# Kernel optimization log

Measured on AMD Instinct MI355X. Metric: run time of the kernel, lower is better.

The kernel has to match this reference:

```python
import jax, jax.numpy as jnp
import numpy as np
import math

B, T, D, H = 2, 2048, 1024, 16


def _layernorm(x, gamma, beta, eps=1e-5):
    mu = jnp.mean(x, axis=-1, keepdims=True)
    var = jnp.var(x, axis=-1, keepdims=True)
    return (x - mu) * jax.lax.rsqrt(var + eps) * gamma + beta


def setup_inputs() -> dict:
    key = jax.random.key(0)
    ks = jax.random.split(key, 12)
    s = 1.0 / math.sqrt(D)
    return {
        "x": jax.random.normal(ks[0], (B, T, D), dtype=jnp.float32),
        "src_mask": jax.random.randint(ks[1], (B, T, T), 0, 2, dtype=jnp.int32),
        "ln_gamma": jnp.ones((D,), jnp.float32),
        "ln_beta": jnp.zeros((D,), jnp.float32),
        "Wq": jax.random.normal(ks[2], (D, D), jnp.float32) * s,
        "bq": jnp.zeros((D,), jnp.float32),
        "Wk": jax.random.normal(ks[3], (D, D), jnp.float32) * s,
        "bk": jnp.zeros((D,), jnp.float32),
        "Wv": jax.random.normal(ks[4], (D, D), jnp.float32) * s,
        "bv": jnp.zeros((D,), jnp.float32),
        "Wo": jax.random.normal(ks[5], (D, D), jnp.float32) * s,
        "bo": jnp.zeros((D,), jnp.float32),
    }


def reference(x, src_mask, ln_gamma, ln_beta, Wq, bq, Wk, bk, Wv, bv, Wo, bo):
    Bx, Tx, Dx = x.shape
    dh = Dx // H
    xn = _layernorm(x, ln_gamma, ln_beta)  # single LN; the three calls are identical
    q = (xn @ Wq + bq).reshape(Bx, Tx, H, dh)
    k = (xn @ Wk + bk).reshape(Bx, Tx, H, dh)
    v = (xn @ Wv + bv).reshape(Bx, Tx, H, dh)
    # scores: B, n, m, h
    attn = jnp.einsum('bnhd,bmhd->bnmh', q, k) / math.sqrt(dh)
    attn = attn + (1.0 - src_mask.astype(attn.dtype))[..., None] * -100000.0
    weight = jax.nn.softmax(attn, axis=2)
    y = jnp.einsum('bnmh,bmhd->bnhd', weight, v).reshape(Bx, Tx, Dx)
    return x + (y @ Wo + bo)
```

## Files before the change

### kernel.cpp

```cpp
#include <hip/hip_runtime.h>
#include <hip/hip_bf16.h>
#include <stdint.h>

#define Tq 2048
#define Dd 1024
#define Hh 16

typedef unsigned short u16;
typedef __attribute__((ext_vector_type(8))) short short8;
typedef __attribute__((ext_vector_type(4))) float f32x4;

__device__ __forceinline__ u16 f2bf(float f) {
  union { float f; unsigned u; } v; v.f = f;
  unsigned r = (v.u + 0x7fffu + ((v.u >> 16) & 1u)) >> 16;
  return (u16)r;
}

__device__ __forceinline__ unsigned pk2bf(float a, float b) {
  __hip_bfloat162 h = __float22bfloat162_rn(float2{a, b});
  union { __hip_bfloat162 h; unsigned u; } c; c.h = h;
  return c.u;
}

__device__ __forceinline__ void load_lds16(const void* g, void* l) {
  __builtin_amdgcn_global_load_lds(
      (const __attribute__((address_space(1))) unsigned*)g,
      (__attribute__((address_space(3))) unsigned*)l, 16, 0, 0);
}

__device__ __forceinline__ f32x4 mfma16(short8 a, short8 b, f32x4 c) {
  return __builtin_amdgcn_mfma_f32_16x16x32_bf16(a, b, c, 0, 0, 0);
}

__global__ __launch_bounds__(256) void prep_kernel(
    const float* __restrict__ x, const float* __restrict__ gamma,
    const float* __restrict__ beta, u16* __restrict__ xn,
    const float* __restrict__ W0, const float* __restrict__ W1,
    const float* __restrict__ W2, const float* __restrict__ W3,
    u16* __restrict__ o_qkv, u16* __restrict__ o_o,
    const int* __restrict__ mask, uint32_t* __restrict__ bits,
    const float* __restrict__ bq, const float* __restrict__ bk,
    const float* __restrict__ bv, float* __restrict__ bias3) {
  __shared__ float t[32][33];
  int idx = blockIdx.x;
  int tid = threadIdx.x;
  if (idx < 4096) {
    int row = idx;
    const float4 v = ((const float4*)(x + (size_t)row * Dd))[tid];
    float s = v.x + v.y + v.z + v.w;
    float s2 = v.x * v.x + v.y * v.y + v.z * v.z + v.w * v.w;
#pragma unroll
    for (int off = 1; off < 64; off <<= 1) {
      s += __shfl_xor(s, off);
      s2 += __shfl_xor(s2, off);
    }
    int w = tid >> 6;
    if ((tid & 63) == 0) { t[0][w] = s; t[0][4 + w] = s2; }
    __syncthreads();
    s = t[0][0] + t[0][1] + t[0][2] + t[0][3];
    s2 = t[0][4] + t[0][5] + t[0][6] + t[0][7];
    float mu = s * (1.0f / Dd);
    float var = s2 * (1.0f / Dd) - mu * mu;
    float rstd = rsqrtf(var + 1e-5f);
    const float4 g = ((const float4*)gamma)[tid];
    const float4 bb = ((const float4*)beta)[tid];
    union { unsigned us[2]; uint2 u2; } o;
    o.us[0] = pk2bf((v.x - mu) * rstd * g.x + bb.x, (v.y - mu) * rstd * g.y + bb.y);
    o.us[1] = pk2bf((v.z - mu) * rstd * g.z + bb.z, (v.w - mu) * rstd * g.w + bb.w);
    *(uint2*)(xn + (size_t)row * Dd + tid * 4) = o.u2;
  } else if (idx < 8192) {
    int ti = idx - 4096;
    int z = ti >> 10, i = ti & 1023;
    const float* W = (z == 0) ? W0 : (z == 1) ? W1 : (z == 2) ? W2 : W3;
    u16* out = (z < 3) ? (o_qkv + (size_t)z * 1024 * 1024) : o_o;
    int k0 = (i & 31) * 32, n0 = (i >> 5) * 32;
    int tx = tid & 31, ty = tid >> 5;
#pragma unroll
    for (int j = 0; j < 4; ++j)
      t[ty + j * 8][tx] = W[(size_t)(k0 + ty + j * 8) * Dd + n0 + tx];
    __syncthreads();
#pragma unroll
    for (int j = 0; j < 4; ++j)
      out[(size_t)(n0 + ty + j * 8) * Dd + k0 + tx] = f2bf(t[tx][ty + j * 8]);
  } else if (idx < 9216) {
    int m = idx - 8192;
    int b = m >> 9, rest = m & 511;
    int qw = rest >> 3, kblk = rest & 7;
    int k = kblk * 256 + tid;
    const int* mp = mask + ((size_t)b * Tq + qw * 32) * Tq + k;
    uint32_t wv = 0;
#pragma unroll
    for (int j = 0; j < 32; ++j) wv |= (mp[(size_t)j * Tq] ? 1u : 0u) << j;
    bits[((size_t)b * 64 + qw) * Tq + k] = wv;
  } else {
    int i = (idx - 9216) * 256 + tid;
    float v = (i < 1024) ? bq[i] : (i < 2048) ? bk[i - 1024] : bv[i - 2048];
    bias3[i] = v;
  }
}

__global__ __launch_bounds__(256) void vt_kernel(
    const u16* __restrict__ qkv, u16* __restrict__ vt) {
  __shared__ u16 t[32][33];
  int bh = blockIdx.z;
  int b = bh >> 4, h = bh & 15;
  int t0 = blockIdx.x * 32, d0 = blockIdx.y * 32;
  int tx = threadIdx.x & 31, ty = threadIdx.x >> 5;
#pragma unroll
  for (int i = 0; i < 4; ++i)
    t[ty + i * 8][tx] =
        qkv[(size_t)(b * Tq + t0 + ty + i * 8) * 3072 + 2048 + h * 64 + d0 + tx];
  __syncthreads();
#pragma unroll
  for (int i = 0; i < 4; ++i)
    vt[((size_t)bh * 64 + d0 + ty + i * 8) * Tq + t0 + tx] = t[tx][ty + i * 8];
}

template <int MODE, int MT>
__global__ __launch_bounds__(256) void gemm_bt(
    const u16* __restrict__ A, const u16* __restrict__ Bt,
    const float* __restrict__ bias, const float* __restrict__ resid,
    void* __restrict__ Cout, int ldc, int K) {
  constexpr int MTI = MT / 32;
  constexpr int ACALLS = MT / 64;
  __shared__ u16 As[MT * 32];
  __shared__ u16 Bs[128 * 32];
  int tid = threadIdx.x;
  int lane = tid & 63, w = tid >> 6;
  int l16 = lane & 15, quad = lane >> 4;
  int wm = w >> 1, wn = w & 1;
  int m0 = blockIdx.y * MT, n0 = blockIdx.x * 128;
  int srow = lane >> 2, scol = (lane & 3) << 3;
  const u16* ga0 = A + (size_t)(m0 + srow) * K + scol;
  const u16* gb0 = Bt + (size_t)(n0 + srow) * K + scol;
  f32x4 acc[MTI][4];
#pragma unroll
  for (int i = 0; i < MTI; ++i)
#pragma unroll
    for (int j = 0; j < 4; ++j) acc[i][j] = {0.f, 0.f, 0.f, 0.f};

  for (int k0 = 0; k0 < K; k0 += 32) {
    __syncthreads();
#pragma unroll
    for (int c = 0; c < ACALLS; ++c) {
      int rb = w * (MT / 4) + c * 16;
      load_lds16(ga0 + (size_t)rb * K + k0, (char*)As + rb * 64);
    }
#pragma unroll
    for (int c = 0; c < 2; ++c) {
      int rb = w * 32 + c * 16;
      load_lds16(gb0 + (size_t)rb * K + k0, (char*)Bs + rb * 64);
    }
    __syncthreads();
    short8 af[MTI], bf[4];
#pragma unroll
    for (int mt = 0; mt < MTI; ++mt)
      af[mt] = *(const short8*)&As[(wm * (MT / 2) + mt * 16 + l16) * 32 + quad * 8];
#pragma unroll
    for (int nt = 0; nt < 4; ++nt)
      bf[nt] = *(const short8*)&Bs[(wn * 64 + nt * 16 + l16) * 32 + quad * 8];
#pragma unroll
    for (int mt = 0; mt < MTI; ++mt)
#pragma unroll
      for (int nt = 0; nt < 4; ++nt)
        acc[mt][nt] = mfma16(af[mt], bf[nt], acc[mt][nt]);
  }
#pragma unroll
  for (int nt = 0; nt < 4; ++nt) {
    int col = n0 + wn * 64 + nt * 16 + l16;
    float bv = bias[col];
    float scl = (MODE == 0 && col < 1024) ? 0.125f : 1.0f;
#pragma unroll
    for (int mt = 0; mt < MTI; ++mt) {
#pragma unroll
      for (int r = 0; r < 4; ++r) {
        int row = m0 + wm * (MT / 2) + mt * 16 + quad * 4 + r;
        size_t idx = (size_t)row * ldc + col;
        float vv = (acc[mt][nt][r] + bv) * scl;
        if (MODE == 0)
          ((u16*)Cout)[idx] = f2bf(vv);
        else
          ((float*)Cout)[idx] = vv + resid[idx];
      }
    }
  }
}

__global__ __launch_bounds__(256, 2) void attn_kernel(
    const u16* __restrict__ qkv, const u16* __restrict__ vt,
    const uint32_t* __restrict__ mbits, u16* __restrict__ ybuf) {
  __shared__ u16 Ks[2][64 * 64];
  __shared__ u16 Vs[2][64 * 64];
  __shared__ u16 Plds[4][32 * 64];
  int tid = threadIdx.x;
  int lane = tid & 63, w = tid >> 6;
  int l16 = lane & 15, quad = lane >> 4;
  int x7 = l16 & 7;
  int qt = blockIdx.x, h = blockIdx.y, b = blockIdx.z;
  int qbase = qt * 128 + w * 32;
  const u16* Qb = qkv + (size_t)b * Tq * 3072 + h * 64;
  const u16* Kb = Qb + 1024;
  const u16* Vb = vt + ((size_t)(b * Hh + h)) * 64 * Tq;
  const uint32_t* Mrow = mbits + ((size_t)b * 64 + (qbase >> 5)) * Tq;
  u16* Pw = Plds[w];

  int half = (w & 1) * 32;
  int r8 = lane >> 3;
  int phys = lane & 7;
  int chunk = phys ^ r8;
  bool isK = (w < 2);

  short8 qf[2][2];
#pragma unroll
  for (int nt = 0; nt < 2; ++nt)
#pragma unroll
    for (int ks = 0; ks < 2; ++ks)
      qf[nt][ks] = *(const short8*)&Qb[(size_t)(qbase + nt * 16 + l16) * 3072 +
                                       ks * 32 + quad * 8];

  f32x4 acc[2][4];
#pragma unroll
  for (int i = 0; i < 2; ++i)
#pragma unroll
    for (int j = 0; j < 4; ++j) acc[i][j] = {0.f, 0.f, 0.f, 0.f};
  float lst[2] = {0.f, 0.f};

  auto stage = [&](int buf, int k0) {
    if (isK) {
#pragma unroll
      for (int j = 0; j < 4; ++j)
        load_lds16(Kb + (size_t)(k0 + half + j * 8 + r8) * 3072 + chunk * 8,
                   (char*)&Ks[buf][0] + (half + j * 8) * 128);
    } else {
#pragma unroll
      for (int j = 0; j < 4; ++j)
        load_lds16(Vb + (size_t)(half + j * 8 + r8) * Tq + k0 + chunk * 8,
                   (char*)&Vs[buf][0] + (half + j * 8) * 128);
    }
  };

  stage(0, 0);

  for (int kt = 0; kt < 32; ++kt) {
    int k0 = kt * 64;
    int buf = kt & 1;
    __syncthreads();
    uint32_t mv[4][4];
#pragma unroll
    for (int mt = 0; mt < 4; ++mt) {
      uint4 m4 = *(const uint4*)&Mrow[k0 + mt * 16 + quad * 4];
      mv[mt][0] = m4.x; mv[mt][1] = m4.y; mv[mt][2] = m4.z; mv[mt][3] = m4.w;
    }
    if (kt < 31) stage(buf ^ 1, k0 + 64);
    const u16* Kt = Ks[buf];
    const u16* Vtile = Vs[buf];
    f32x4 s[4][2];
#pragma unroll
    for (int i = 0; i < 4; ++i)
#pragma unroll
      for (int j = 0; j < 2; ++j) s[i][j] = {0.f, 0.f, 0.f, 0.f};
#pragma unroll
    for (int mt = 0; mt < 4; ++mt)
#pragma unroll
      for (int ks = 0; ks < 2; ++ks) {
        short8 kf = *(const short8*)&Kt[(mt * 16 + l16) * 64 +
                                        (((ks << 2) | quad) ^ x7) * 8];
#pragma unroll
        for (int nt = 0; nt < 2; ++nt)
          s[mt][nt] = mfma16(kf, qf[nt][ks], s[mt][nt]);
      }
#pragma unroll
    for (int nt = 0; nt < 2; ++nt) {
      int shift = nt * 16 + l16;
#pragma unroll
      for (int mt = 0; mt < 4; ++mt) {
#pragma unroll
        for (int r = 0; r < 4; ++r) {
          float sv = ((mv[mt][r] >> shift) & 1u) ? s[mt][nt][r] : -100000.0f;
          float p = __expf(sv);
          s[mt][nt][r] = p;
          lst[nt] += p;
        }
        union { unsigned us[2]; uint2 u2; } pk;
        pk.us[0] = pk2bf(s[mt][nt][0], s[mt][nt][1]);
        pk.us[1] = pk2bf(s[mt][nt][2], s[mt][nt][3]);
        int p16 = (mt * 2 + (quad >> 1)) ^ x7;
        *(uint2*)&Pw[(nt * 16 + l16) * 64 + p16 * 8 + (quad & 1) * 4] = pk.u2;
      }
    }
    short8 pf[2][2];
#pragma unroll
    for (int mt2 = 0; mt2 < 2; ++mt2)
#pragma unroll
      for (int ks = 0; ks < 2; ++ks)
        pf[mt2][ks] = *(const short8*)&Pw[(mt2 * 16 + l16) * 64 +
                                          (((ks << 2) | quad) ^ x7) * 8];
#pragma unroll
    for (int ks = 0; ks < 2; ++ks)
#pragma unroll
      for (int nt2 = 0; nt2 < 4; ++nt2) {
        short8 vf = *(const short8*)&Vtile[(nt2 * 16 + l16) * 64 +
                                           (((ks << 2) | quad) ^ x7) * 8];
#pragma unroll
        for (int mt2 = 0; mt2 < 2; ++mt2)
          acc[mt2][nt2] = mfma16(pf[mt2][ks], vf, acc[mt2][nt2]);
      }
  }
#pragma unroll
  for (int nt = 0; nt < 2; ++nt) {
    lst[nt] += __shfl_xor(lst[nt], 16);
    lst[nt] += __shfl_xor(lst[nt], 32);
  }
#pragma unroll
  for (int mt2 = 0; mt2 < 2; ++mt2)
#pragma unroll
    for (int r = 0; r < 4; ++r) {
      float li = 1.0f / __shfl(lst[mt2], quad * 4 + r);
      size_t row = (size_t)b * Tq + qbase + mt2 * 16 + quad * 4 + r;
#pragma unroll
      for (int nt2 = 0; nt2 < 4; ++nt2)
        ybuf[row * Dd + h * 64 + nt2 * 16 + l16] = f2bf(acc[mt2][nt2][r] * li);
    }
}

extern "C" void kernel_launch(void* const* d_in, const int* in_sizes, int n_in,
                              void* d_out, int out_size, void* d_ws, size_t ws_size,
                              hipStream_t stream) {
  (void)in_sizes; (void)n_in; (void)out_size; (void)ws_size;
  const float* x = (const float*)d_in[0];
  const int* mask = (const int*)d_in[1];
  const float* gamma = (const float*)d_in[2];
  const float* beta = (const float*)d_in[3];
  const float* Wq = (const float*)d_in[4];
  const float* bq = (const float*)d_in[5];
  const float* Wk = (const float*)d_in[6];
  const float* bk = (const float*)d_in[7];
  const float* Wv = (const float*)d_in[8];
  const float* bv = (const float*)d_in[9];
  const float* Wo = (const float*)d_in[10];
  const float* bo = (const float*)d_in[11];
  float* out = (float*)d_out;
  char* ws = (char*)d_ws;

  constexpr size_t SZ_XN = (size_t)4096 * 1024 * 2;
  constexpr size_t SZ_WTQ = (size_t)3072 * 1024 * 2;
  constexpr size_t SZ_WOT = (size_t)1024 * 1024 * 2;
  constexpr size_t SZ_B3 = 3072 * 4;
  constexpr size_t SZ_QKV = (size_t)4096 * 3072 * 2;
  constexpr size_t SZ_MBITS = (size_t)2 * 64 * 2048 * 4;
  constexpr size_t SZ_VT = (size_t)2 * 16 * 64 * 2048 * 2;
  size_t off = 0;
  u16* xn = (u16*)(ws + off); off += SZ_XN;
  u16* wtqkv = (u16*)(ws + off); off += SZ_WTQ;
  u16* wot = (u16*)(ws + off); off += SZ_WOT;
  float* bias3 = (float*)(ws + off); off += SZ_B3;
  u16* qkvb = (u16*)(ws + off); off += SZ_QKV;
  uint32_t* mbits = (uint32_t*)(ws + off); off += SZ_MBITS;
  u16* vtb = (u16*)(ws + off); off += SZ_VT;
  u16* ybuf = (u16*)(ws + off);

  prep_kernel<<<dim3(9228), dim3(256), 0, stream>>>(
      x, gamma, beta, xn, Wq, Wk, Wv, Wo, wtqkv, wot, mask, mbits, bq, bk, bv,
      bias3);
  gemm_bt<0, 128><<<dim3(24, 32), dim3(256), 0, stream>>>(
      xn, wtqkv, bias3, nullptr, qkvb, 3072, 1024);
  vt_kernel<<<dim3(64, 2, 32), dim3(256), 0, stream>>>(qkvb, vtb);
  attn_kernel<<<dim3(16, 16, 2), dim3(256), 0, stream>>>(qkvb, vtb, mbits, ybuf);
  gemm_bt<1, 64><<<dim3(8, 64), dim3(256), 0, stream>>>(
      ybuf, wot, bo, x, out, 1024, 1024);
}
```

Measured before the change: 245.5 us.

## Halve attention query tile per block, use exp2 with folded scale and bitmask select

```diff
diff --git a/kernel.cpp b/kernel.cpp
--- a/kernel.cpp
+++ b/kernel.cpp
@@ -169,7 +169,7 @@
   for (int nt = 0; nt < 4; ++nt) {
     int col = n0 + wn * 64 + nt * 16 + l16;
     float bv = bias[col];
-    float scl = (MODE == 0 && col < 1024) ? 0.125f : 1.0f;
+    float scl = (MODE == 0 && col < 1024) ? 0.18033688011112042f : 1.0f;
 #pragma unroll
     for (int mt = 0; mt < MTI; ++mt) {
 #pragma unroll
@@ -186,22 +186,24 @@
   }
 }
 
-__global__ __launch_bounds__(256, 2) void attn_kernel(
+__global__ __launch_bounds__(256, 4) void attn_kernel(
     const u16* __restrict__ qkv, const u16* __restrict__ vt,
     const uint32_t* __restrict__ mbits, u16* __restrict__ ybuf) {
   __shared__ u16 Ks[2][64 * 64];
   __shared__ u16 Vs[2][64 * 64];
-  __shared__ u16 Plds[4][32 * 64];
+  __shared__ u16 Plds[4][16 * 64];
   int tid = threadIdx.x;
   int lane = tid & 63, w = tid >> 6;
   int l16 = lane & 15, quad = lane >> 4;
   int x7 = l16 & 7;
   int qt = blockIdx.x, h = blockIdx.y, b = blockIdx.z;
-  int qbase = qt * 128 + w * 32;
+  int qbase = qt * 64 + w * 16;
   const u16* Qb = qkv + (size_t)b * Tq * 3072 + h * 64;
   const u16* Kb = Qb + 1024;
   const u16* Vb = vt + ((size_t)(b * Hh + h)) * 64 * Tq;
   const uint32_t* Mrow = mbits + ((size_t)b * 64 + (qbase >> 5)) * Tq;
+  int shift = (qbase & 31) + l16;
+  int shl = 31 - shift;
   u16* Pw = Plds[w];
 
   int half = (w & 1) * 32;
@@ -210,20 +212,15 @@
   int chunk = phys ^ r8;
   bool isK = (w < 2);
 
-  short8 qf[2][2];
-#pragma unroll
-  for (int nt = 0; nt < 2; ++nt)
-#pragma unroll
-    for (int ks = 0; ks < 2; ++ks)
-      qf[nt][ks] = *(const short8*)&Qb[(size_t)(qbase + nt * 16 + l16) * 3072 +
-                                       ks * 32 + quad * 8];
-
-  f32x4 acc[2][4];
-#pragma unroll
-  for (int i = 0; i < 2; ++i)
-#pragma unroll
-    for (int j = 0; j < 4; ++j) acc[i][j] = {0.f, 0.f, 0.f, 0.f};
-  float lst[2] = {0.f, 0.f};
+  short8 qf[2];
+#pragma unroll
+  for (int ks = 0; ks < 2; ++ks)
+    qf[ks] = *(const short8*)&Qb[(size_t)(qbase + l16) * 3072 + ks * 32 + quad * 8];
+
+  f32x4 acc[4];
+#pragma unroll
+  for (int j = 0; j < 4; ++j) acc[j] = {0.f, 0.f, 0.f, 0.f};
+  float lsa[4] = {0.f, 0.f, 0.f, 0.f};
 
   auto stage = [&](int buf, int k0) {
     if (isK) {
@@ -254,73 +251,57 @@
     if (kt < 31) stage(buf ^ 1, k0 + 64);
     const u16* Kt = Ks[buf];
     const u16* Vtile = Vs[buf];
-    f32x4 s[4][2];
-#pragma unroll
-    for (int i = 0; i < 4; ++i)
-#pragma unroll
-      for (int j = 0; j < 2; ++j) s[i][j] = {0.f, 0.f, 0.f, 0.f};
+    f32x4 s[4];
+#pragma unroll
+    for (int i = 0; i < 4; ++i) s[i] = {0.f, 0.f, 0.f, 0.f};
 #pragma unroll
     for (int mt = 0; mt < 4; ++mt)
 #pragma unroll
       for (int ks = 0; ks < 2; ++ks) {
         short8 kf = *(const short8*)&Kt[(mt * 16 + l16) * 64 +
                                         (((ks << 2) | quad) ^ x7) * 8];
-#pragma unroll
-        for (int nt = 0; nt < 2; ++nt)
-          s[mt][nt] = mfma16(kf, qf[nt][ks], s[mt][nt]);
+        s[mt] = mfma16(kf, qf[ks], s[mt]);
       }
 #pragma unroll
-    for (int nt = 0; nt < 2; ++nt) {
-      int shift = nt * 16 + l16;
-#pragma unroll
-      for (int mt = 0; mt < 4; ++mt) {
-#pragma unroll
-        for (int r = 0; r < 4; ++r) {
-          float sv = ((mv[mt][r] >> shift) & 1u) ? s[mt][nt][r] : -100000.0f;
-          float p = __expf(sv);
-          s[mt][nt][r] = p;
-          lst[nt] += p;
-        }
-        union { unsigned us[2]; uint2 u2; } pk;
-        pk.us[0] = pk2bf(s[mt][nt][0], s[mt][nt][1]);
-        pk.us[1] = pk2bf(s[mt][nt][2], s[mt][nt][3]);
-        int p16 = (mt * 2 + (quad >> 1)) ^ x7;
-        *(uint2*)&Pw[(nt * 16 + l16) * 64 + p16 * 8 + (quad & 1) * 4] = pk.u2;
+    for (int mt = 0; mt < 4; ++mt) {
+#pragma unroll
+      for (int r = 0; r < 4; ++r) {
+        float p = __builtin_amdgcn_exp2f(s[mt][r]);
+        int keep = (int)(mv[mt][r] << shl) >> 31;
+        union { float f; int i; } u; u.f = p; u.i &= keep;
+        s[mt][r] = u.f;
+        lsa[r] += u.f;
       }
-    }
-    short8 pf[2][2];
-#pragma unroll
-    for (int mt2 = 0; mt2 < 2; ++mt2)
-#pragma unroll
-      for (int ks = 0; ks < 2; ++ks)
-        pf[mt2][ks] = *(const short8*)&Pw[(mt2 * 16 + l16) * 64 +
-                                          (((ks << 2) | quad) ^ x7) * 8];
+      union { unsigned us[2]; uint2 u2; } pk;
+      pk.us[0] = pk2bf(s[mt][0], s[mt][1]);
+      pk.us[1] = pk2bf(s[mt][2], s[mt][3]);
+      int p16 = (mt * 2 + (quad >> 1)) ^ x7;
+      *(uint2*)&Pw[l16 * 64 + p16 * 8 + (quad & 1) * 4] = pk.u2;
+    }
+    short8 pf[2];
+#pragma unroll
+    for (int ks = 0; ks < 2; ++ks)
+      pf[ks] = *(const short8*)&Pw[l16 * 64 + (((ks << 2) | quad) ^ x7) * 8];
 #pragma unroll
     for (int ks = 0; ks < 2; ++ks)
 #pragma unroll
       for (int nt2 = 0; nt2 < 4; ++nt2) {
         short8 vf = *(const short8*)&Vtile[(nt2 * 16 + l16) * 64 +
                                            (((ks << 2) | quad) ^ x7) * 8];
-#pragma unroll
-        for (int mt2 = 0; mt2 < 2; ++mt2)
-          acc[mt2][nt2] = mfma16(pf[mt2][ks], vf, acc[mt2][nt2]);
+        acc[nt2] = mfma16(pf[ks], vf, acc[nt2]);
       }
   }
-#pragma unroll
-  for (int nt = 0; nt < 2; ++nt) {
-    lst[nt] += __shfl_xor(lst[nt], 16);
-    lst[nt] += __shfl_xor(lst[nt], 32);
-  }
-#pragma unroll
-  for (int mt2 = 0; mt2 < 2; ++mt2)
-#pragma unroll
-    for (int r = 0; r < 4; ++r) {
-      float li = 1.0f / __shfl(lst[mt2], quad * 4 + r);
-      size_t row = (size_t)b * Tq + qbase + mt2 * 16 + quad * 4 + r;
-#pragma unroll
-      for (int nt2 = 0; nt2 < 4; ++nt2)
-        ybuf[row * Dd + h * 64 + nt2 * 16 + l16] = f2bf(acc[mt2][nt2][r] * li);
-    }
+  float lst = (lsa[0] + lsa[1]) + (lsa[2] + lsa[3]);
+  lst += __shfl_xor(lst, 16);
+  lst += __shfl_xor(lst, 32);
+#pragma unroll
+  for (int r = 0; r < 4; ++r) {
+    float li = 1.0f / __shfl(lst, quad * 4 + r);
+    size_t row = (size_t)b * Tq + qbase + quad * 4 + r;
+#pragma unroll
+    for (int nt2 = 0; nt2 < 4; ++nt2)
+      ybuf[row * Dd + h * 64 + nt2 * 16 + l16] = f2bf(acc[nt2][r] * li);
+  }
 }
 
 extern "C" void kernel_launch(void* const* d_in, const int* in_sizes, int n_in,
@@ -365,7 +346,7 @@
   gemm_bt<0, 128><<<dim3(24, 32), dim3(256), 0, stream>>>(
       xn, wtqkv, bias3, nullptr, qkvb, 3072, 1024);
   vt_kernel<<<dim3(64, 2, 32), dim3(256), 0, stream>>>(qkvb, vtb);
-  attn_kernel<<<dim3(16, 16, 2), dim3(256), 0, stream>>>(qkvb, vtb, mbits, ybuf);
+  attn_kernel<<<dim3(32, 16, 2), dim3(256), 0, stream>>>(qkvb, vtb, mbits, ybuf);
   gemm_bt<1, 64><<<dim3(8, 64), dim3(256), 0, stream>>>(
       ybuf, wot, bo, x, out, 1024, 1024);
 }
```

Result: no change. 246.3 us (+0.3%).
